# Kernel tuning notes

Hardware: AMD Instinct MI355X
Metric: run time of the kernel (lower is better)

## Reference

```python
import jax, jax.numpy as jnp
import numpy as np

B, N, C_IN = 4, 8192, 64
NPOINT, NSAMPLE = 2048, 32
RADIUS = 0.8


def fps(xyz, npoint):
    """Furthest point sampling. xyz: (B, N, 3) -> (B, npoint) int32 indices."""
    b, n, _ = xyz.shape
    init_idx = jnp.zeros((b,), jnp.int32)
    dists0 = jnp.full((b, n), 1e10, xyz.dtype)

    def body(carry, _):
        dists, last = carry
        p = xyz[jnp.arange(b), last]                      # (B, 3) last selected point
        d = jnp.sum((xyz - p[:, None, :]) ** 2, axis=-1)  # (B, N)
        dists = jnp.minimum(dists, d)
        nxt = jnp.argmax(dists, axis=-1).astype(jnp.int32)
        return (dists, nxt), nxt

    (_, _), rest = jax.lax.scan(body, (dists0, init_idx), None, length=npoint - 1)
    return jnp.concatenate([init_idx[None, :], rest], axis=0).T  # (B, npoint)


def setup_inputs() -> dict:
    key = jax.random.key(0)
    k = jax.random.split(key, 4)
    xyz = jax.random.normal(k[0], (B, N, 3), jnp.float32) * 3.0   # point coords
    features = jax.random.normal(k[1], (B, C_IN, N), jnp.float32)
    w1 = jax.random.normal(k[2], (128, C_IN + 3), jnp.float32) * 0.05
    b1 = jnp.zeros((128,), jnp.float32)
    w2 = jax.random.normal(k[3], (256, 128), jnp.float32) * 0.05
    b2 = jnp.zeros((256,), jnp.float32)
    return {"xyz": xyz, "features": features, "w1": w1, "b1": b1, "w2": w2, "b2": b2}


def reference(xyz, features, w1, b1, w2, b2):
    b, n, _ = xyz.shape
    # --- d-fps sampling + gather_operation(new_xyz) ---
    idx_fps = fps(xyz, NPOINT)                                  # (B, S)
    new_xyz = jax.vmap(lambda p, i: p[i])(xyz, idx_fps)         # (B, S, 3)

    # --- ball query (QueryAndGroup): first NSAMPLE points within RADIUS ---
    d2 = jnp.sum((new_xyz[:, :, None, :] - xyz[:, None, :, :]) ** 2, -1)  # (B, S, N)
    in_ball = d2 < RADIUS ** 2
    idx_cnt = jnp.sum(in_ball, axis=-1)                          # (B, S)
    score = jnp.where(in_ball, jnp.arange(n, dtype=jnp.int32), n)
    neg_vals, _ = jax.lax.top_k(-score, NSAMPLE)
    idx = -neg_vals                                              # (B, S, ns) smallest valid indices
    valid = idx < n
    first = jnp.where(valid[..., :1], idx[..., :1], 0)           # pad empties with first hit (or 0)
    idx = jnp.where(valid, idx, first)

    # --- group: relative xyz concat features (use_xyz=True) ---
    gxyz = jax.vmap(lambda p, i: p[i])(xyz, idx)                 # (B, S, ns, 3)
    rel = (gxyz - new_xyz[:, :, None, :]).transpose(0, 3, 1, 2)  # (B, 3, S, ns)
    gfeat = jax.vmap(lambda f, i: f[:, i])(features, idx)        # (B, C, S, ns)
    g = jnp.concatenate([rel, gfeat], axis=1)                    # (B, C+3, S, ns)
    g = g * (idx_cnt > 0).astype(g.dtype)[:, None, :, None]      # zero empty balls

    # --- shared point MLP (1x1 conv stack) + max pool over samples ---
    h = jax.nn.relu(jnp.einsum('oc,bcsn->bosn', w1, g) + b1[None, :, None, None])
    h = jax.nn.relu(jnp.einsum('oc,bcsn->bosn', w2, h) + b2[None, :, None, None])
    pooled = jnp.max(h, axis=-1)                                 # (B, 256, S)
    return new_xyz, pooled
```

## Files before the change

### kernel.cpp

```cpp
#include <hip/hip_runtime.h>

#define NPTS   8192
#define NPT    2048
#define NS     32
#define CIN    64
#define BATCH  4
#define R2     0.64f

#define NWORK  252
#define NQUAD  2048

__global__ __launch_bounds__(256) void prep_kernel(const float* __restrict__ w1,
                                                   const float* __restrict__ w2,
                                                   float* __restrict__ w1t,
                                                   float* __restrict__ w2t) {
  int i = blockIdx.x * 256 + threadIdx.x;
  if (i < 128 * 67) {
    int o = i / 67, c = i % 67;
    w1t[c * 128 + o] = w1[i];
  }
  if (i < 256 * 128) {
    int o = i >> 7, c = i & 127;
    w2t[c * 256 + o] = w2[i];
  }
}

__global__ __launch_bounds__(256) void prep_t_kernel(const float* __restrict__ feat,
                                                     float* __restrict__ FT) {
  const int b = blockIdx.x >> 7;
  const int n0 = (blockIdx.x & 127) << 6;
  const int tid = threadIdx.x;
  __shared__ float T[64][65];

  const float* F = feat + (size_t)b * CIN * NPTS;
#pragma unroll
  for (int p = 0; p < 16; ++p) {
    int c = p * 4 + (tid >> 6), ln = tid & 63;
    T[c][ln] = F[(size_t)c * NPTS + n0 + ln];
  }
  __syncthreads();
  float* O = FT + (size_t)b * NPTS * CIN;
#pragma unroll
  for (int p = 0; p < 4; ++p) {
    int j = tid >> 2, q = (tid & 3) + p * 4;
    float4 v = make_float4(T[q * 4 + 0][j], T[q * 4 + 1][j],
                           T[q * 4 + 2][j], T[q * 4 + 3][j]);
    *(float4*)&O[(size_t)(n0 + j) * CIN + q * 4] = v;
  }
}

__device__ inline uint32_t part1by2(uint32_t x) {
  x &= 1023u;
  x = (x | (x << 16)) & 0x030000FFu;
  x = (x | (x << 8))  & 0x0300F00Fu;
  x = (x | (x << 4))  & 0x030C30C3u;
  x = (x | (x << 2))  & 0x09249249u;
  return x;
}

__device__ inline uint32_t morton3(float x, float y, float z) {
  int qx = (int)((x + 16.f) * 32.f);
  int qy = (int)((y + 16.f) * 32.f);
  int qz = (int)((z + 16.f) * 32.f);
  qx = qx < 0 ? 0 : (qx > 1023 ? 1023 : qx);
  qy = qy < 0 ? 0 : (qy > 1023 ? 1023 : qy);
  qz = qz < 0 ? 0 : (qz > 1023 ? 1023 : qz);
  return part1by2((uint32_t)qx) | (part1by2((uint32_t)qy) << 1) | (part1by2((uint32_t)qz) << 2);
}

__global__ __launch_bounds__(1024) void sort_kernel(const float* __restrict__ xyz,
                                                    float4* __restrict__ sorted) {
  const int b = blockIdx.x;
  const int tid = threadIdx.x;
  const float* X = xyz + (size_t)b * NPTS * 3;
  __shared__ uint32_t S[NPTS];

  for (int k = 0; k < 8; ++k) {
    int p = tid + (k << 10);
    uint32_t m = morton3(X[p * 3 + 0], X[p * 3 + 1], X[p * 3 + 2]);
    S[p] = ((m >> 11) << 13) | (uint32_t)p;
  }
  __syncthreads();
  for (unsigned k = 2; k <= NPTS; k <<= 1) {
    for (unsigned j = k >> 1; j > 0; j >>= 1) {
      for (int i = tid; i < NPTS; i += 1024) {
        int l = i ^ (int)j;
        if (l > i) {
          uint32_t a = S[i], c = S[l];
          bool sw = ((i & k) == 0) ? (a > c) : (a < c);
          if (sw) { S[i] = c; S[l] = a; }
        }
      }
      __syncthreads();
    }
  }
  for (int k = 0; k < 8; ++k) {
    int pos = tid + (k << 10);
    int o = (int)(S[pos] & 8191u);
    float4 v;
    v.x = X[o * 3 + 0]; v.y = X[o * 3 + 1]; v.z = X[o * 3 + 2];
    v.w = __int_as_float(o);
    sorted[(size_t)b * NPTS + pos] = v;
  }
}


#define DPP_ROR_U32_MAX(v)                                                       \
  {                                                                              \
    uint32_t _t;                                                                 \
    _t = (uint32_t)__builtin_amdgcn_update_dpp(0, (int)(v), 0x121, 0xF, 0xF, false); if (_t > (v)) (v) = _t; \
    _t = (uint32_t)__builtin_amdgcn_update_dpp(0, (int)(v), 0x122, 0xF, 0xF, false); if (_t > (v)) (v) = _t; \
    _t = (uint32_t)__builtin_amdgcn_update_dpp(0, (int)(v), 0x124, 0xF, 0xF, false); if (_t > (v)) (v) = _t; \
    _t = (uint32_t)__builtin_amdgcn_update_dpp(0, (int)(v), 0x128, 0xF, 0xF, false); if (_t > (v)) (v) = _t; \
  }

#define DPP_ROR_U32_MIN(v)                                                       \
  {                                                                              \
    uint32_t _t;                                                                 \
    _t = (uint32_t)__builtin_amdgcn_update_dpp(-1, (int)(v), 0x121, 0xF, 0xF, false); if (_t < (v)) (v) = _t; \
    _t = (uint32_t)__builtin_amdgcn_update_dpp(-1, (int)(v), 0x122, 0xF, 0xF, false); if (_t < (v)) (v) = _t; \
    _t = (uint32_t)__builtin_amdgcn_update_dpp(-1, (int)(v), 0x124, 0xF, 0xF, false); if (_t < (v)) (v) = _t; \
    _t = (uint32_t)__builtin_amdgcn_update_dpp(-1, (int)(v), 0x128, 0xF, 0xF, false); if (_t < (v)) (v) = _t; \
  }

#define CSWAP(i, j)                                                              \
  if (oid[i] > oid[j]) {                                                         \
    int _ti = oid[i]; oid[i] = oid[j]; oid[j] = _ti;                             \
    float _tf;                                                                   \
    _tf = px[i]; px[i] = px[j]; px[j] = _tf;                                     \
    _tf = py[i]; py[i] = py[j]; py[j] = _tf;                                     \
    _tf = pz[i]; pz[i] = pz[j]; pz[j] = _tf;                                     \
  }

__global__ __launch_bounds__(1024, 1) void fused_kernel(
    const float* __restrict__ xyz, const float4* __restrict__ sorted,
    const float* __restrict__ FT,
    const float* __restrict__ w1t, const float* __restrict__ b1,
    const float* __restrict__ w2t, const float* __restrict__ b2,
    float* __restrict__ new_xyz, float* __restrict__ pooled,
    int* __restrict__ progress) {
  const int tid = threadIdx.x;
  const int lane = tid & 63;
  const int wv = tid >> 6;

  __shared__ __align__(16) char SM[100416];

  if (blockIdx.x < 4) {
    const int b = blockIdx.x;
    float* XL = (float*)SM;
    uint2 (*rec)[16] = (uint2(*)[16])(SM + 98304);
    const float* X = xyz + (size_t)b * NPTS * 3;
    const float4* SP = sorted + (size_t)b * NPTS;

    for (int i = tid; i < NPTS * 3; i += 1024) XL[i] = X[i];

    float px[8], py[8], pz[8], dmin[8];
    int oid[8];
#pragma unroll
    for (int k = 0; k < 8; ++k) {
      float4 p = SP[tid * 8 + k];
      px[k] = p.x; py[k] = p.y; pz[k] = p.z;
      oid[k] = __float_as_int(p.w);
      dmin[k] = 1e10f;
    }
    CSWAP(0, 1) CSWAP(2, 3) CSWAP(4, 5) CSWAP(6, 7)
    CSWAP(0, 2) CSWAP(1, 3) CSWAP(4, 6) CSWAP(5, 7)
    CSWAP(1, 2) CSWAP(5, 6)
    CSWAP(0, 4) CSWAP(1, 5) CSWAP(2, 6) CSWAP(3, 7)
    CSWAP(2, 4) CSWAP(3, 5)
    CSWAP(1, 2) CSWAP(3, 4) CSWAP(5, 6)

    float bxmin = px[0], bxmax = px[0], bymin = py[0], bymax = py[0], bzmin = pz[0], bzmax = pz[0];
#pragma unroll
    for (int k = 1; k < 8; ++k) {
      bxmin = fminf(bxmin, px[k]); bxmax = fmaxf(bxmax, px[k]);
      bymin = fminf(bymin, py[k]); bymax = fmaxf(bymax, py[k]);
      bzmin = fminf(bzmin, pz[k]); bzmax = fmaxf(bzmax, pz[k]);
    }
    float cmaxv = 1e10f;
    int   cmaxi = oid[0];
    uint32_t wwm = 0u, wwi = 0u;

    float cx = X[0], cy = X[1], cz = X[2];
    if (tid == 0) {
      new_xyz[(size_t)b * NPT * 3 + 0] = cx;
      new_xyz[(size_t)b * NPT * 3 + 1] = cy;
      new_xyz[(size_t)b * NPT * 3 + 2] = cz;
    }
    __syncthreads();

    for (int t = 1; t < NPT; ++t) {
      float ex = fmaxf(fmaxf(bxmin - cx, cx - bxmax), 0.f);
      float ey = fmaxf(fmaxf(bymin - cy, cy - bymax), 0.f);
      float ez = fmaxf(fmaxf(bzmin - cz, cz - bzmax), 0.f);
      float dlb = (ex * ex + ey * ey + ez * ez) * 0.9999f;
      bool act = dlb < cmaxv;

      if (__ballot(act)) {
        if (act) {
          float mv = -1.0f; int mi = 0;
#pragma unroll
          for (int k = 0; k < 8; ++k) {
            float dx = px[k] - cx, dy = py[k] - cy, dz = pz[k] - cz;
            float d = __fadd_rn(__fadd_rn(__fmul_rn(dx, dx), __fmul_rn(dy, dy)), __fmul_rn(dz, dz));
            float dm = fminf(dmin[k], d);
            dmin[k] = dm;
            if (dm > mv) { mv = dm; mi = oid[k]; }
          }
          cmaxv = mv; cmaxi = mi;
        }
        uint32_t vb = __float_as_uint(cmaxv);
        uint32_t rm = vb;
        DPP_ROR_U32_MAX(rm)
        uint32_t m0 = (uint32_t)__builtin_amdgcn_readlane((int)rm, 0);
        uint32_t m1 = (uint32_t)__builtin_amdgcn_readlane((int)rm, 16);
        uint32_t m2 = (uint32_t)__builtin_amdgcn_readlane((int)rm, 32);
        uint32_t m3 = (uint32_t)__builtin_amdgcn_readlane((int)rm, 48);
        uint32_t wm = m0 > m1 ? m0 : m1;
        uint32_t wmb = m2 > m3 ? m2 : m3;
        wm = wm > wmb ? wm : wmb;
        unsigned long long em = __ballot(vb == wm);
        uint32_t wi;
        if (__popcll(em) == 1) {
          wi = (uint32_t)__builtin_amdgcn_readlane(cmaxi, __ffsll(em) - 1);
        } else {
          uint32_t ik = (vb == wm) ? (uint32_t)cmaxi : 0xFFFFFFFFu;
          DPP_ROR_U32_MIN(ik)
          uint32_t i0 = (uint32_t)__builtin_amdgcn_readlane((int)ik, 0);
          uint32_t i1 = (uint32_t)__builtin_amdgcn_readlane((int)ik, 16);
          uint32_t i2 = (uint32_t)__builtin_amdgcn_readlane((int)ik, 32);
          uint32_t i3 = (uint32_t)__builtin_amdgcn_readlane((int)ik, 48);
          wi = i0 < i1 ? i0 : i1;
          uint32_t wib = i2 < i3 ? i2 : i3;
          wi = wi < wib ? wi : wib;
        }
        wwm = wm; wwi = wi;
      }

      const int buf = t & 1;
      if (lane == 0) { rec[buf][wv].x = wwm; rec[buf][wv].y = wwi; }
      __syncthreads();

      uint2 r = rec[buf][lane & 15];
      uint32_t bm = r.x;
      DPP_ROR_U32_MAX(bm)
      uint32_t ci = (r.x == bm) ? r.y : 0xFFFFFFFFu;
      DPP_ROR_U32_MIN(ci)
      int sidx = __builtin_amdgcn_readfirstlane((int)ci);

      cx = XL[3 * sidx + 0];
      cy = XL[3 * sidx + 1];
      cz = XL[3 * sidx + 2];

      if (tid == 0) {
        float* o = new_xyz + ((size_t)b * NPT + t) * 3;
        o[0] = cx; o[1] = cy; o[2] = cz;
        if ((t & 15) == 15)
          __hip_atomic_store(progress + b, t, __ATOMIC_RELEASE, __HIP_MEMORY_SCOPE_AGENT);
      }
    }
  } else {
    float* G    = (float*)SM;
    float* H1   = (float*)(SM + 34304);
    int*   lidx = (int*)(SM + 99840);
    float* ctr  = (float*)(SM + 100352);

    const int wbid = blockIdx.x - 4;

    for (int qg = wbid; qg < NQUAD; qg += NWORK) {
      const int b = qg & 3;
      const int s0 = (qg >> 2) * 4;
      const float* X  = xyz + (size_t)b * NPTS * 3;
      const float* Fp = FT + (size_t)b * NPTS * CIN;

      if (tid == 0) {
        while (__hip_atomic_load(progress + b, __ATOMIC_ACQUIRE, __HIP_MEMORY_SCOPE_AGENT) < s0 + 3)
          __builtin_amdgcn_s_sleep(2);
      }
      __syncthreads();

      if (tid < 12) ctr[tid] = new_xyz[((size_t)b * NPT + s0) * 3 + tid];
      if (wv < 4) {
        const int s = s0 + wv;
        const float cx = new_xyz[((size_t)b * NPT + s) * 3 + 0];
        const float cy = new_xyz[((size_t)b * NPT + s) * 3 + 1];
        const float cz = new_xyz[((size_t)b * NPT + s) * 3 + 2];
        int* out = lidx + wv * NS;
        int found = 0;
        int first = -1;
        for (int base = 0; base < NPTS; base += 64) {
          const int p = base + lane;
          float x = X[p * 3 + 0], y = X[p * 3 + 1], z = X[p * 3 + 2];
          float dx = x - cx, dy = y - cy, dz = z - cz;
          float d2 = __fadd_rn(__fadd_rn(__fmul_rn(dx, dx), __fmul_rn(dy, dy)), __fmul_rn(dz, dz));
          unsigned long long mask = __ballot(d2 < R2);
          if (mask != 0ull && first < 0) first = base + __ffsll((unsigned long long)mask) - 1;
          if (found < NS) {
            if ((mask >> lane) & 1ull) {
              int rank = found + __popcll(mask & ((1ull << lane) - 1ull));
              if (rank < NS) out[rank] = p;
            }
          }
          found += __popcll(mask);
          if (found >= NS) break;
        }
        if (found < NS) {
          int pad = (first < 0) ? 0 : first;
          if (lane >= found && lane < NS) out[lane] = pad;
        }
      }
      __syncthreads();

      {
        int j = tid >> 3, q = tid & 7;
        int p = lidx[j];
        const float4* row = (const float4*)(Fp + (size_t)p * CIN);
        float4 v0 = row[q * 2 + 0];
        float4 v1 = row[q * 2 + 1];
        float vs[8] = {v0.x, v0.y, v0.z, v0.w, v1.x, v1.y, v1.z, v1.w};
#pragma unroll
        for (int i = 0; i < 8; ++i)
          G[(3 + q * 8 + i) * 128 + j] = vs[i];
      }
      if (tid < 384) {
        int c = tid >> 7, j = tid & 127;
        int p = lidx[j];
        G[c * 128 + j] = X[p * 3 + c] - ctr[(j >> 5) * 3 + c];
      }
      __syncthreads();

      {
        const int oi = tid >> 5, ji = tid & 31;
        const int o0 = oi * 4, j0 = ji * 4;
        float acc[4][4];
#pragma unroll
        for (int i = 0; i < 4; ++i)
#pragma unroll
          for (int jj = 0; jj < 4; ++jj) acc[i][jj] = 0.f;
#pragma unroll 4
        for (int c = 0; c < 67; ++c) {
          float4 g  = *(const float4*)&G[c * 128 + j0];
          float4 wf = *(const float4*)&w1t[c * 128 + o0];
          float ga[4] = {g.x, g.y, g.z, g.w};
          float wa[4] = {wf.x, wf.y, wf.z, wf.w};
#pragma unroll
          for (int i = 0; i < 4; ++i)
#pragma unroll
            for (int jj = 0; jj < 4; ++jj)
              acc[i][jj] = fmaf(wa[i], ga[jj], acc[i][jj]);
        }
        float4 bb = *(const float4*)&b1[o0];
        float ba[4] = {bb.x, bb.y, bb.z, bb.w};
#pragma unroll
        for (int i = 0; i < 4; ++i) {
          float4 h;
          h.x = fmaxf(acc[i][0] + ba[i], 0.f);
          h.y = fmaxf(acc[i][1] + ba[i], 0.f);
          h.z = fmaxf(acc[i][2] + ba[i], 0.f);
          h.w = fmaxf(acc[i][3] + ba[i], 0.f);
          *(float4*)&H1[(o0 + i) * 128 + j0] = h;
        }
      }
      __syncthreads();

      {
        const int oi = tid >> 5, ji = tid & 31;
        const int o0 = oi * 8, j0 = ji * 4;
        float acc[8][4];
#pragma unroll
        for (int i = 0; i < 8; ++i)
#pragma unroll
          for (int jj = 0; jj < 4; ++jj) acc[i][jj] = 0.f;
#pragma unroll 2
        for (int c = 0; c < 128; ++c) {
          float4 h  = *(const float4*)&H1[c * 128 + j0];
          float4 wa4 = *(const float4*)&w2t[c * 256 + o0];
          float4 wb4 = *(const float4*)&w2t[c * 256 + o0 + 4];
          float ha[4] = {h.x, h.y, h.z, h.w};
          float wa[8] = {wa4.x, wa4.y, wa4.z, wa4.w, wb4.x, wb4.y, wb4.z, wb4.w};
#pragma unroll
          for (int i = 0; i < 8; ++i)
#pragma unroll
            for (int jj = 0; jj < 4; ++jj)
              acc[i][jj] = fmaf(wa[i], ha[jj], acc[i][jj]);
        }
        float4 b2a = *(const float4*)&b2[o0];
        float4 b2b = *(const float4*)&b2[o0 + 4];
        float bb[8] = {b2a.x, b2a.y, b2a.z, b2a.w, b2b.x, b2b.y, b2b.z, b2b.w};
        float m[8];
#pragma unroll
        for (int i = 0; i < 8; ++i) {
          float v0 = fmaxf(acc[i][0] + bb[i], 0.f);
          float v1 = fmaxf(acc[i][1] + bb[i], 0.f);
          float v2 = fmaxf(acc[i][2] + bb[i], 0.f);
          float v3 = fmaxf(acc[i][3] + bb[i], 0.f);
          m[i] = fmaxf(fmaxf(v0, v1), fmaxf(v2, v3));
        }
#pragma unroll
        for (int off = 1; off < 8; off <<= 1)
#pragma unroll
          for (int i = 0; i < 8; ++i) m[i] = fmaxf(m[i], __shfl_xor(m[i], off));
        if ((ji & 7) == 0) {
          int sidx = s0 + (ji >> 3);
#pragma unroll
          for (int i = 0; i < 8; ++i)
            pooled[((size_t)b * 256 + o0 + i) * (size_t)NPT + sidx] = m[i];
        }
      }
    }
  }
}

extern "C" void kernel_launch(void* const* d_in, const int* in_sizes, int n_in,
                              void* d_out, int out_size, void* d_ws, size_t ws_size,
                              hipStream_t stream) {
  (void)in_sizes; (void)n_in; (void)out_size; (void)ws_size;
  const float* xyz  = (const float*)d_in[0];
  const float* feat = (const float*)d_in[1];
  const float* w1   = (const float*)d_in[2];
  const float* b1   = (const float*)d_in[3];
  const float* w2   = (const float*)d_in[4];
  const float* b2   = (const float*)d_in[5];

  float* out     = (float*)d_out;
  float* new_xyz = out;
  float* pooled  = out + (size_t)BATCH * NPT * 3;

  char* ws = (char*)d_ws;
  float*  w1t      = (float*)ws;
  float*  w2t      = (float*)(ws + 34304);
  float4* sorted   = (float4*)(ws + 165376);
  float*  FT       = (float*)(ws + 689664);
  int*    progress = (int*)(ws + 9078272);

  prep_kernel<<<128, 256, 0, stream>>>(w1, w2, w1t, w2t);
  prep_t_kernel<<<BATCH * 128, 256, 0, stream>>>(feat, FT);
  sort_kernel<<<BATCH, 1024, 0, stream>>>(xyz, sorted);
  (void)hipMemsetAsync(progress, 0, 16, stream);
  fused_kernel<<<256, 1024, 0, stream>>>(xyz, sorted, FT, w1t, b1, w2t, b2,
                                         new_xyz, pooled, progress);
}
```

Measured before the change: 1.685 ms.

## Add wave-level bounding-box skip and broadcast winner coords via LDS records

In the FPS blocks, each wave now computes a wave-wide bounding box and skips the whole per-thread check and the wave reduction when that box cannot beat the wave's previous max. The winning lane also writes its point coordinates into a small per-wave LDS record, and the next centre is picked out of those records with readlane. This replaces the indexed lookup into a 96KB copy of xyz held in LDS, which is removed along with its initial load. The cost is more bookkeeping per iteration, and the correctness of the skip depends on the stale wave max staying a valid bound.

```diff
diff --git a/kernel.cpp b/kernel.cpp
--- a/kernel.cpp
+++ b/kernel.cpp
@@ -147,12 +147,10 @@
 
   if (blockIdx.x < 4) {
     const int b = blockIdx.x;
-    float* XL = (float*)SM;
-    uint2 (*rec)[16] = (uint2(*)[16])(SM + 98304);
+    uint2  (*rec)[16]  = (uint2(*)[16])(SM + 98304);
+    float4 (*recc)[16] = (float4(*)[16])(SM + 98560);
     const float* X = xyz + (size_t)b * NPTS * 3;
     const float4* SP = sorted + (size_t)b * NPTS;
-
-    for (int i = tid; i < NPTS * 3; i += 1024) XL[i] = X[i];
 
     float px[8], py[8], pz[8], dmin[8];
     int oid[8];
@@ -177,9 +175,25 @@
       bymin = fminf(bymin, py[k]); bymax = fmaxf(bymax, py[k]);
       bzmin = fminf(bzmin, pz[k]); bzmax = fmaxf(bzmax, pz[k]);
     }
+    float wbxmin = bxmin, wbxmax = bxmax;
+    float wbymin = bymin, wbymax = bymax;
+    float wbzmin = bzmin, wbzmax = bzmax;
+#pragma unroll
+    for (int off = 1; off < 64; off <<= 1) {
+      wbxmin = fminf(wbxmin, __shfl_xor(wbxmin, off));
+      wbxmax = fmaxf(wbxmax, __shfl_xor(wbxmax, off));
+      wbymin = fminf(wbymin, __shfl_xor(wbymin, off));
+      wbymax = fmaxf(wbymax, __shfl_xor(wbymax, off));
+      wbzmin = fminf(wbzmin, __shfl_xor(wbzmin, off));
+      wbzmax = fmaxf(wbzmax, __shfl_xor(wbzmax, off));
+    }
+
     float cmaxv = 1e10f;
     int   cmaxi = oid[0];
     uint32_t wwm = 0u, wwi = 0u;
+    float wwmf = 1e10f;
+    bool  iswin = false;
+    float wwx = 0.f, wwy = 0.f, wwz = 0.f;
 
     float cx = X[0], cy = X[1], cz = X[2];
     if (tid == 0) {
@@ -190,67 +204,83 @@
     __syncthreads();
 
     for (int t = 1; t < NPT; ++t) {
-      float ex = fmaxf(fmaxf(bxmin - cx, cx - bxmax), 0.f);
-      float ey = fmaxf(fmaxf(bymin - cy, cy - bymax), 0.f);
-      float ez = fmaxf(fmaxf(bzmin - cz, cz - bzmax), 0.f);
-      float dlb = (ex * ex + ey * ey + ez * ez) * 0.9999f;
-      bool act = dlb < cmaxv;
-
-      if (__ballot(act)) {
-        if (act) {
-          float mv = -1.0f; int mi = 0;
-#pragma unroll
-          for (int k = 0; k < 8; ++k) {
-            float dx = px[k] - cx, dy = py[k] - cy, dz = pz[k] - cz;
-            float d = __fadd_rn(__fadd_rn(__fmul_rn(dx, dx), __fmul_rn(dy, dy)), __fmul_rn(dz, dz));
-            float dm = fminf(dmin[k], d);
-            dmin[k] = dm;
-            if (dm > mv) { mv = dm; mi = oid[k]; }
+      float exw = fmaxf(fmaxf(wbxmin - cx, cx - wbxmax), 0.f);
+      float eyw = fmaxf(fmaxf(wbymin - cy, cy - wbymax), 0.f);
+      float ezw = fmaxf(fmaxf(wbzmin - cz, cz - wbzmax), 0.f);
+      float dlbw = (exw * exw + eyw * eyw + ezw * ezw) * 0.9999f;
+
+      if (dlbw < wwmf) {
+        float ex = fmaxf(fmaxf(bxmin - cx, cx - bxmax), 0.f);
+        float ey = fmaxf(fmaxf(bymin - cy, cy - bymax), 0.f);
+        float ez = fmaxf(fmaxf(bzmin - cz, cz - bzmax), 0.f);
+        float dlb = (ex * ex + ey * ey + ez * ez) * 0.9999f;
+        bool act = dlb < cmaxv;
+
+        if (__ballot(act)) {
+          if (act) {
+            float mv = -1.0f; int mi = 0;
+#pragma unroll
+            for (int k = 0; k < 8; ++k) {
+              float dx = px[k] - cx, dy = py[k] - cy, dz = pz[k] - cz;
+              float d = __fadd_rn(__fadd_rn(__fmul_rn(dx, dx), __fmul_rn(dy, dy)), __fmul_rn(dz, dz));
+              float dm = fminf(dmin[k], d);
+              dmin[k] = dm;
+              if (dm > mv) { mv = dm; mi = oid[k]; }
+            }
+            cmaxv = mv; cmaxi = mi;
           }
-          cmaxv = mv; cmaxi = mi;
-        }
-        uint32_t vb = __float_as_uint(cmaxv);
-        uint32_t rm = vb;
-        DPP_ROR_U32_MAX(rm)
-        uint32_t m0 = (uint32_t)__builtin_amdgcn_readlane((int)rm, 0);
-        uint32_t m1 = (uint32_t)__builtin_amdgcn_readlane((int)rm, 16);
-        uint32_t m2 = (uint32_t)__builtin_amdgcn_readlane((int)rm, 32);
-        uint32_t m3 = (uint32_t)__builtin_amdgcn_readlane((int)rm, 48);
-        uint32_t wm = m0 > m1 ? m0 : m1;
-        uint32_t wmb = m2 > m3 ? m2 : m3;
-        wm = wm > wmb ? wm : wmb;
-        unsigned long long em = __ballot(vb == wm);
-        uint32_t wi;
-        if (__popcll(em) == 1) {
-          wi = (uint32_t)__builtin_amdgcn_readlane(cmaxi, __ffsll(em) - 1);
-        } else {
-          uint32_t ik = (vb == wm) ? (uint32_t)cmaxi : 0xFFFFFFFFu;
-          DPP_ROR_U32_MIN(ik)
-          uint32_t i0 = (uint32_t)__builtin_amdgcn_readlane((int)ik, 0);
-          uint32_t i1 = (uint32_t)__builtin_amdgcn_readlane((int)ik, 16);
-          uint32_t i2 = (uint32_t)__builtin_amdgcn_readlane((int)ik, 32);
-          uint32_t i3 = (uint32_t)__builtin_amdgcn_readlane((int)ik, 48);
-          wi = i0 < i1 ? i0 : i1;
-          uint32_t wib = i2 < i3 ? i2 : i3;
-          wi = wi < wib ? wi : wib;
-        }
-        wwm = wm; wwi = wi;
+          uint32_t vb = __float_as_uint(cmaxv);
+          uint32_t rm = vb;
+          DPP_ROR_U32_MAX(rm)
+          uint32_t m0 = (uint32_t)__builtin_amdgcn_readlane((int)rm, 0);
+          uint32_t m1 = (uint32_t)__builtin_amdgcn_readlane((int)rm, 16);
+          uint32_t m2 = (uint32_t)__builtin_amdgcn_readlane((int)rm, 32);
+          uint32_t m3 = (uint32_t)__builtin_amdgcn_readlane((int)rm, 48);
+          uint32_t wm = m0 > m1 ? m0 : m1;
+          uint32_t wmb = m2 > m3 ? m2 : m3;
+          wm = wm > wmb ? wm : wmb;
+          unsigned long long em = __ballot(vb == wm);
+          uint32_t wi;
+          if (__popcll(em) == 1) {
+            wi = (uint32_t)__builtin_amdgcn_readlane(cmaxi, __ffsll(em) - 1);
+          } else {
+            uint32_t ik = (vb == wm) ? (uint32_t)cmaxi : 0xFFFFFFFFu;
+            DPP_ROR_U32_MIN(ik)
+            uint32_t i0 = (uint32_t)__builtin_amdgcn_readlane((int)ik, 0);
+            uint32_t i1 = (uint32_t)__builtin_amdgcn_readlane((int)ik, 16);
+            uint32_t i2 = (uint32_t)__builtin_amdgcn_readlane((int)ik, 32);
+            uint32_t i3 = (uint32_t)__builtin_amdgcn_readlane((int)ik, 48);
+            wi = i0 < i1 ? i0 : i1;
+            uint32_t wib = i2 < i3 ? i2 : i3;
+            wi = wi < wib ? wi : wib;
+          }
+          wwm = wm; wwi = wi;
+          wwmf = __uint_as_float(wm);
+          iswin = (vb == wm) && ((uint32_t)cmaxi == wi);
+          if (iswin) {
+#pragma unroll
+            for (int k = 0; k < 8; ++k)
+              if (oid[k] == (int)wi) { wwx = px[k]; wwy = py[k]; wwz = pz[k]; }
+          }
+        }
       }
 
       const int buf = t & 1;
       if (lane == 0) { rec[buf][wv].x = wwm; rec[buf][wv].y = wwi; }
-      __syncthreads();
-
-      uint2 r = rec[buf][lane & 15];
+      if (iswin)     { recc[buf][wv] = make_float4(wwx, wwy, wwz, 0.f); }
+      __syncthreads();
+
+      uint2  r  = rec[buf][lane & 15];
+      float4 rc = recc[buf][lane & 15];
       uint32_t bm = r.x;
       DPP_ROR_U32_MAX(bm)
-      uint32_t ci = (r.x == bm) ? r.y : 0xFFFFFFFFu;
+      uint32_t ci = (r.x == bm) ? ((r.y << 4) | (uint32_t)(lane & 15)) : 0xFFFFFFFFu;
       DPP_ROR_U32_MIN(ci)
-      int sidx = __builtin_amdgcn_readfirstlane((int)ci);
-
-      cx = XL[3 * sidx + 0];
-      cy = XL[3 * sidx + 1];
-      cz = XL[3 * sidx + 2];
+      int s = __builtin_amdgcn_readfirstlane((int)ci);
+      int wl = s & 15;
+      cx = __int_as_float(__builtin_amdgcn_readlane(__float_as_int(rc.x), wl));
+      cy = __int_as_float(__builtin_amdgcn_readlane(__float_as_int(rc.y), wl));
+      cz = __int_as_float(__builtin_amdgcn_readlane(__float_as_int(rc.z), wl));
 
       if (tid == 0) {
         float* o = new_xyz + ((size_t)b * NPT + t) * 3;
```

Result: slower. 2.558 ms (+51.8%).

## Fold prep, transpose and Morton sort kernels into the persistent fused kernel

Applied to the files above, without the earlier changes.

Removes three separate launches by moving the weight transpose and feature transpose into the worker blocks and the Morton bitonic sort into the FPS blocks, using shared memory instead of a global sorted buffer. Worker blocks synchronize on a global counter before consuming FT. FPS results are staged in a shared ring and flushed to global memory every 16 steps. This cuts launch overhead and lets the sort overlap with the transposes, at the cost of more shared memory per block and a grid-wide spin barrier that assumes all blocks are co-resident.

```diff
diff --git a/kernel.cpp b/kernel.cpp
--- a/kernel.cpp
+++ b/kernel.cpp
@@ -9,45 +9,6 @@
 
 #define NWORK  252
 #define NQUAD  2048
-
-__global__ __launch_bounds__(256) void prep_kernel(const float* __restrict__ w1,
-                                                   const float* __restrict__ w2,
-                                                   float* __restrict__ w1t,
-                                                   float* __restrict__ w2t) {
-  int i = blockIdx.x * 256 + threadIdx.x;
-  if (i < 128 * 67) {
-    int o = i / 67, c = i % 67;
-    w1t[c * 128 + o] = w1[i];
-  }
-  if (i < 256 * 128) {
-    int o = i >> 7, c = i & 127;
-    w2t[c * 256 + o] = w2[i];
-  }
-}
-
-__global__ __launch_bounds__(256) void prep_t_kernel(const float* __restrict__ feat,
-                                                     float* __restrict__ FT) {
-  const int b = blockIdx.x >> 7;
-  const int n0 = (blockIdx.x & 127) << 6;
-  const int tid = threadIdx.x;
-  __shared__ float T[64][65];
-
-  const float* F = feat + (size_t)b * CIN * NPTS;
-#pragma unroll
-  for (int p = 0; p < 16; ++p) {
-    int c = p * 4 + (tid >> 6), ln = tid & 63;
-    T[c][ln] = F[(size_t)c * NPTS + n0 + ln];
-  }
-  __syncthreads();
-  float* O = FT + (size_t)b * NPTS * CIN;
-#pragma unroll
-  for (int p = 0; p < 4; ++p) {
-    int j = tid >> 2, q = (tid & 3) + p * 4;
-    float4 v = make_float4(T[q * 4 + 0][j], T[q * 4 + 1][j],
-                           T[q * 4 + 2][j], T[q * 4 + 3][j]);
-    *(float4*)&O[(size_t)(n0 + j) * CIN + q * 4] = v;
-  }
-}
 
 __device__ inline uint32_t part1by2(uint32_t x) {
   x &= 1023u;
@@ -68,42 +29,6 @@
   return part1by2((uint32_t)qx) | (part1by2((uint32_t)qy) << 1) | (part1by2((uint32_t)qz) << 2);
 }
 
-__global__ __launch_bounds__(1024) void sort_kernel(const float* __restrict__ xyz,
-                                                    float4* __restrict__ sorted) {
-  const int b = blockIdx.x;
-  const int tid = threadIdx.x;
-  const float* X = xyz + (size_t)b * NPTS * 3;
-  __shared__ uint32_t S[NPTS];
-
-  for (int k = 0; k < 8; ++k) {
-    int p = tid + (k << 10);
-    uint32_t m = morton3(X[p * 3 + 0], X[p * 3 + 1], X[p * 3 + 2]);
-    S[p] = ((m >> 11) << 13) | (uint32_t)p;
-  }
-  __syncthreads();
-  for (unsigned k = 2; k <= NPTS; k <<= 1) {
-    for (unsigned j = k >> 1; j > 0; j >>= 1) {
-      for (int i = tid; i < NPTS; i += 1024) {
-        int l = i ^ (int)j;
-        if (l > i) {
-          uint32_t a = S[i], c = S[l];
-          bool sw = ((i & k) == 0) ? (a > c) : (a < c);
-          if (sw) { S[i] = c; S[l] = a; }
-        }
-      }
-      __syncthreads();
-    }
-  }
-  for (int k = 0; k < 8; ++k) {
-    int pos = tid + (k << 10);
-    int o = (int)(S[pos] & 8191u);
-    float4 v;
-    v.x = X[o * 3 + 0]; v.y = X[o * 3 + 1]; v.z = X[o * 3 + 2];
-    v.w = __int_as_float(o);
-    sorted[(size_t)b * NPTS + pos] = v;
-  }
-}
-
 
 #define DPP_ROR_U32_MAX(v)                                                       \
   {                                                                              \
@@ -133,34 +58,57 @@
   }
 
 __global__ __launch_bounds__(1024, 1) void fused_kernel(
-    const float* __restrict__ xyz, const float4* __restrict__ sorted,
-    const float* __restrict__ FT,
-    const float* __restrict__ w1t, const float* __restrict__ b1,
-    const float* __restrict__ w2t, const float* __restrict__ b2,
+    const float* __restrict__ xyz, const float* __restrict__ feat,
+    const float* __restrict__ w1, const float* __restrict__ b1,
+    const float* __restrict__ w2, const float* __restrict__ b2,
+    float* __restrict__ w1t, float* __restrict__ w2t,
+    float* __restrict__ FT,
     float* __restrict__ new_xyz, float* __restrict__ pooled,
     int* __restrict__ progress) {
   const int tid = threadIdx.x;
   const int lane = tid & 63;
   const int wv = tid >> 6;
-
-  __shared__ __align__(16) char SM[100416];
+  int* ftflag = progress + 4;
+
+  __shared__ __align__(16) char SM[131520];
 
   if (blockIdx.x < 4) {
     const int b = blockIdx.x;
-    float* XL = (float*)SM;
-    uint2 (*rec)[16] = (uint2(*)[16])(SM + 98304);
+    float*     XL  = (float*)SM;
+    uint32_t*  S   = (uint32_t*)(SM + 98304);
+    uint2 (*rec)[16] = (uint2(*)[16])(SM + 131072);
+    float*     ring = (float*)(SM + 131328);
     const float* X = xyz + (size_t)b * NPTS * 3;
-    const float4* SP = sorted + (size_t)b * NPTS;
 
     for (int i = tid; i < NPTS * 3; i += 1024) XL[i] = X[i];
+    __syncthreads();
+    for (int k = 0; k < 8; ++k) {
+      int p = tid + (k << 10);
+      uint32_t m = morton3(XL[p * 3 + 0], XL[p * 3 + 1], XL[p * 3 + 2]);
+      S[p] = ((m >> 11) << 13) | (uint32_t)p;
+    }
+    __syncthreads();
+    for (unsigned kk = 2; kk <= NPTS; kk <<= 1) {
+      for (unsigned j = kk >> 1; j > 0; j >>= 1) {
+        for (int i = tid; i < NPTS; i += 1024) {
+          int l = i ^ (int)j;
+          if (l > i) {
+            uint32_t a = S[i], c = S[l];
+            bool sw = ((i & kk) == 0) ? (a > c) : (a < c);
+            if (sw) { S[i] = c; S[l] = a; }
+          }
+        }
+        __syncthreads();
+      }
+    }
 
     float px[8], py[8], pz[8], dmin[8];
     int oid[8];
 #pragma unroll
     for (int k = 0; k < 8; ++k) {
-      float4 p = SP[tid * 8 + k];
-      px[k] = p.x; py[k] = p.y; pz[k] = p.z;
-      oid[k] = __float_as_int(p.w);
+      int o = (int)(S[tid * 8 + k] & 8191u);
+      px[k] = XL[3 * o + 0]; py[k] = XL[3 * o + 1]; pz[k] = XL[3 * o + 2];
+      oid[k] = o;
       dmin[k] = 1e10f;
     }
     CSWAP(0, 1) CSWAP(2, 3) CSWAP(4, 5) CSWAP(6, 7)
@@ -181,13 +129,8 @@
     int   cmaxi = oid[0];
     uint32_t wwm = 0u, wwi = 0u;
 
-    float cx = X[0], cy = X[1], cz = X[2];
-    if (tid == 0) {
-      new_xyz[(size_t)b * NPT * 3 + 0] = cx;
-      new_xyz[(size_t)b * NPT * 3 + 1] = cy;
-      new_xyz[(size_t)b * NPT * 3 + 2] = cz;
-    }
-    __syncthreads();
+    float cx = XL[0], cy = XL[1], cz = XL[2];
+    if (tid == 0) { ring[0] = cx; ring[1] = cy; ring[2] = cz; }
 
     for (int t = 1; t < NPT; ++t) {
       float ex = fmaxf(fmaxf(bxmin - cx, cx - bxmax), 0.f);
@@ -253,10 +196,15 @@
       cz = XL[3 * sidx + 2];
 
       if (tid == 0) {
-        float* o = new_xyz + ((size_t)b * NPT + t) * 3;
-        o[0] = cx; o[1] = cy; o[2] = cz;
-        if ((t & 15) == 15)
+        float* rg = ring + (t & 15) * 3;
+        rg[0] = cx; rg[1] = cy; rg[2] = cz;
+        if ((t & 15) == 15) {
+          float4* dst = (float4*)(new_xyz + ((size_t)b * NPT + (t - 15)) * 3);
+          float4* src = (float4*)ring;
+#pragma unroll
+          for (int q = 0; q < 12; ++q) dst[q] = src[q];
           __hip_atomic_store(progress + b, t, __ATOMIC_RELEASE, __HIP_MEMORY_SCOPE_AGENT);
+        }
       }
     }
   } else {
@@ -266,6 +214,46 @@
     float* ctr  = (float*)(SM + 100352);
 
     const int wbid = blockIdx.x - 4;
+
+    {
+      if (wbid == 0) {
+        for (int i = tid; i < 128 * 67; i += 1024) {
+          int o = i / 67, c = i % 67;
+          w1t[c * 128 + o] = w1[i];
+        }
+        for (int i = tid; i < 256 * 128; i += 1024) {
+          int o = i >> 7, c = i & 127;
+          w2t[c * 256 + o] = w2[i];
+        }
+      }
+      float (*T)[65] = (float(*)[65])SM;
+      for (int tile = wbid; tile < 512; tile += NWORK) {
+        const int tb = tile >> 7;
+        const int n0 = (tile & 127) << 6;
+        const float* F = feat + (size_t)tb * CIN * NPTS;
+        float* O = FT + (size_t)tb * NPTS * CIN;
+#pragma unroll
+        for (int p = 0; p < 4; ++p) {
+          int c = p * 16 + (tid >> 6), ln = tid & 63;
+          T[c][ln] = F[(size_t)c * NPTS + n0 + ln];
+        }
+        __syncthreads();
+        {
+          int j = tid >> 4, q = tid & 15;
+          float4 v = make_float4(T[q * 4 + 0][j], T[q * 4 + 1][j],
+                                 T[q * 4 + 2][j], T[q * 4 + 3][j]);
+          *(float4*)&O[(size_t)(n0 + j) * CIN + q * 4] = v;
+        }
+        __syncthreads();
+      }
+      if (tid == 0)
+        (void)__hip_atomic_fetch_add(ftflag, 1, __ATOMIC_RELEASE, __HIP_MEMORY_SCOPE_AGENT);
+      if (tid == 0) {
+        while (__hip_atomic_load(ftflag, __ATOMIC_ACQUIRE, __HIP_MEMORY_SCOPE_AGENT) < NWORK)
+          __builtin_amdgcn_s_sleep(2);
+      }
+      __syncthreads();
+    }
 
     for (int qg = wbid; qg < NQUAD; qg += NWORK) {
       const int b = qg & 3;
@@ -427,16 +415,12 @@
   float* pooled  = out + (size_t)BATCH * NPT * 3;
 
   char* ws = (char*)d_ws;
-  float*  w1t      = (float*)ws;
-  float*  w2t      = (float*)(ws + 34304);
-  float4* sorted   = (float4*)(ws + 165376);
-  float*  FT       = (float*)(ws + 689664);
-  int*    progress = (int*)(ws + 9078272);
-
-  prep_kernel<<<128, 256, 0, stream>>>(w1, w2, w1t, w2t);
-  prep_t_kernel<<<BATCH * 128, 256, 0, stream>>>(feat, FT);
-  sort_kernel<<<BATCH, 1024, 0, stream>>>(xyz, sorted);
-  (void)hipMemsetAsync(progress, 0, 16, stream);
-  fused_kernel<<<256, 1024, 0, stream>>>(xyz, sorted, FT, w1t, b1, w2t, b2,
-                                         new_xyz, pooled, progress);
+  float* w1t      = (float*)ws;
+  float* w2t      = (float*)(ws + 34304);
+  float* FT       = (float*)(ws + 165376);
+  int*   progress = (int*)(ws + 8553984);
+
+  (void)hipMemsetAsync(progress, 0, 32, stream);
+  fused_kernel<<<256, 1024, 0, stream>>>(xyz, feat, w1, b1, w2, b2,
+                                         w1t, w2t, FT, new_xyz, pooled, progress);
 }
```

Result: no change. 1.704 ms (+1.1%).

## Halve fused kernel block size to 512 threads and double per-thread work

Applied to the files above, without the earlier changes.

Launches the fused kernel with 512 threads per block instead of 1024. Each FPS thread now holds 16 sorted points, merged with an extra sorting network, and the MLP stages compute twice as many output channels per thread. Per-wave FPS records are duplicated into 16 slots so the existing 16-lane reduction still works with 8 waves. The intent is to cut the per-iteration block barrier and reduction cost in the serial FPS loop and allow more blocks per CU. The cost is higher register pressure and less parallelism inside each block for the grouping/MLP phase.

```diff
diff --git a/kernel.cpp b/kernel.cpp
--- a/kernel.cpp
+++ b/kernel.cpp
@@ -132,7 +132,9 @@
     _tf = pz[i]; pz[i] = pz[j]; pz[j] = _tf;                                     \
   }
 
-__global__ __launch_bounds__(1024, 1) void fused_kernel(
+__global__ __launch_bounds__(512)
+__attribute__((amdgpu_waves_per_eu(2, 8)))
+void fused_kernel(
     const float* __restrict__ xyz, const float4* __restrict__ sorted,
     const float* __restrict__ FT,
     const float* __restrict__ w1t, const float* __restrict__ b1,
@@ -143,7 +145,7 @@
   const int lane = tid & 63;
   const int wv = tid >> 6;
 
-  __shared__ __align__(16) char SM[100416];
+  __shared__ __align__(16) char SM[100864];
 
   if (blockIdx.x < 4) {
     const int b = blockIdx.x;
@@ -152,16 +154,15 @@
     const float* X = xyz + (size_t)b * NPTS * 3;
     const float4* SP = sorted + (size_t)b * NPTS;
 
-    for (int i = tid; i < NPTS * 3; i += 1024) XL[i] = X[i];
-
-    float px[8], py[8], pz[8], dmin[8];
-    int oid[8];
-#pragma unroll
-    for (int k = 0; k < 8; ++k) {
-      float4 p = SP[tid * 8 + k];
+    for (int i = tid; i < NPTS * 3; i += 512) XL[i] = X[i];
+
+    float px[16], py[16], pz[16], dmin[16];
+    int oid[16];
+#pragma unroll
+    for (int k = 0; k < 16; ++k) {
+      float4 p = SP[tid * 16 + k];
       px[k] = p.x; py[k] = p.y; pz[k] = p.z;
       oid[k] = __float_as_int(p.w);
-      dmin[k] = 1e10f;
     }
     CSWAP(0, 1) CSWAP(2, 3) CSWAP(4, 5) CSWAP(6, 7)
     CSWAP(0, 2) CSWAP(1, 3) CSWAP(4, 6) CSWAP(5, 7)
@@ -170,9 +171,33 @@
     CSWAP(2, 4) CSWAP(3, 5)
     CSWAP(1, 2) CSWAP(3, 4) CSWAP(5, 6)
 
+    CSWAP(8, 9) CSWAP(10, 11) CSWAP(12, 13) CSWAP(14, 15)
+    CSWAP(8, 10) CSWAP(9, 11) CSWAP(12, 14) CSWAP(13, 15)
+    CSWAP(9, 10) CSWAP(13, 14)
+    CSWAP(8, 12) CSWAP(9, 13) CSWAP(10, 14) CSWAP(11, 15)
+    CSWAP(10, 12) CSWAP(11, 13)
+    CSWAP(9, 10) CSWAP(11, 12) CSWAP(13, 14)
+
+    CSWAP(0, 15) CSWAP(1, 14) CSWAP(2, 13) CSWAP(3, 12)
+    CSWAP(4, 11) CSWAP(5, 10) CSWAP(6, 9) CSWAP(7, 8)
+    CSWAP(0, 4) CSWAP(1, 5) CSWAP(2, 6) CSWAP(3, 7)
+    CSWAP(8, 12) CSWAP(9, 13) CSWAP(10, 14) CSWAP(11, 15)
+    CSWAP(0, 2) CSWAP(1, 3) CSWAP(4, 6) CSWAP(5, 7)
+    CSWAP(8, 10) CSWAP(9, 11) CSWAP(12, 14) CSWAP(13, 15)
+    CSWAP(0, 1) CSWAP(2, 3) CSWAP(4, 5) CSWAP(6, 7)
+    CSWAP(8, 9) CSWAP(10, 11) CSWAP(12, 13) CSWAP(14, 15)
+
+#pragma unroll
+    for (int k = 0; k < 16; ++k) {
+      asm volatile("" : "+v"(px[k]), "+v"(py[k]), "+v"(pz[k]), "+v"(oid[k]));
+    }
+
+#pragma unroll
+    for (int k = 0; k < 16; ++k) dmin[k] = 1e10f;
+
     float bxmin = px[0], bxmax = px[0], bymin = py[0], bymax = py[0], bzmin = pz[0], bzmax = pz[0];
 #pragma unroll
-    for (int k = 1; k < 8; ++k) {
+    for (int k = 1; k < 16; ++k) {
       bxmin = fminf(bxmin, px[k]); bxmax = fmaxf(bxmax, px[k]);
       bymin = fminf(bymin, py[k]); bymax = fmaxf(bymax, py[k]);
       bzmin = fminf(bzmin, pz[k]); bzmax = fmaxf(bzmax, pz[k]);
@@ -200,7 +225,7 @@
         if (act) {
           float mv = -1.0f; int mi = 0;
 #pragma unroll
-          for (int k = 0; k < 8; ++k) {
+          for (int k = 0; k < 16; ++k) {
             float dx = px[k] - cx, dy = py[k] - cy, dz = pz[k] - cz;
             float d = __fadd_rn(__fadd_rn(__fmul_rn(dx, dx), __fmul_rn(dy, dy)), __fmul_rn(dz, dz));
             float dm = fminf(dmin[k], d);
@@ -238,7 +263,10 @@
       }
 
       const int buf = t & 1;
-      if (lane == 0) { rec[buf][wv].x = wwm; rec[buf][wv].y = wwi; }
+      if (lane == 0) {
+        rec[buf][wv].x = wwm;     rec[buf][wv].y = wwi;
+        rec[buf][wv + 8].x = wwm; rec[buf][wv + 8].y = wwi;
+      }
       __syncthreads();
 
       uint2 r = rec[buf][lane & 15];
@@ -312,15 +340,17 @@
       __syncthreads();
 
       {
-        int j = tid >> 3, q = tid & 7;
+        int j = tid >> 2, q = tid & 3;
         int p = lidx[j];
         const float4* row = (const float4*)(Fp + (size_t)p * CIN);
-        float4 v0 = row[q * 2 + 0];
-        float4 v1 = row[q * 2 + 1];
-        float vs[8] = {v0.x, v0.y, v0.z, v0.w, v1.x, v1.y, v1.z, v1.w};
-#pragma unroll
-        for (int i = 0; i < 8; ++i)
-          G[(3 + q * 8 + i) * 128 + j] = vs[i];
+#pragma unroll
+        for (int h = 0; h < 4; ++h) {
+          float4 v = row[q * 4 + h];
+          G[(3 + q * 16 + h * 4 + 0) * 128 + j] = v.x;
+          G[(3 + q * 16 + h * 4 + 1) * 128 + j] = v.y;
+          G[(3 + q * 16 + h * 4 + 2) * 128 + j] = v.z;
+          G[(3 + q * 16 + h * 4 + 3) * 128 + j] = v.w;
+        }
       }
       if (tid < 384) {
         int c = tid >> 7, j = tid & 127;
@@ -331,28 +361,30 @@
 
       {
         const int oi = tid >> 5, ji = tid & 31;
-        const int o0 = oi * 4, j0 = ji * 4;
-        float acc[4][4];
-#pragma unroll
-        for (int i = 0; i < 4; ++i)
+        const int o0 = oi * 8, j0 = ji * 4;
+        float acc[8][4];
+#pragma unroll
+        for (int i = 0; i < 8; ++i)
 #pragma unroll
           for (int jj = 0; jj < 4; ++jj) acc[i][jj] = 0.f;
 #pragma unroll 4
         for (int c = 0; c < 67; ++c) {
           float4 g  = *(const float4*)&G[c * 128 + j0];
-          float4 wf = *(const float4*)&w1t[c * 128 + o0];
+          float4 wa4 = *(const float4*)&w1t[c * 128 + o0];
+          float4 wb4 = *(const float4*)&w1t[c * 128 + o0 + 4];
           float ga[4] = {g.x, g.y, g.z, g.w};
-          float wa[4] = {wf.x, wf.y, wf.z, wf.w};
-#pragma unroll
-          for (int i = 0; i < 4; ++i)
+          float wa[8] = {wa4.x, wa4.y, wa4.z, wa4.w, wb4.x, wb4.y, wb4.z, wb4.w};
+#pragma unroll
+          for (int i = 0; i < 8; ++i)
 #pragma unroll
             for (int jj = 0; jj < 4; ++jj)
               acc[i][jj] = fmaf(wa[i], ga[jj], acc[i][jj]);
         }
-        float4 bb = *(const float4*)&b1[o0];
-        float ba[4] = {bb.x, bb.y, bb.z, bb.w};
-#pragma unroll
-        for (int i = 0; i < 4; ++i) {
+        float4 ba4 = *(const float4*)&b1[o0];
+        float4 bb4 = *(const float4*)&b1[o0 + 4];
+        float ba[8] = {ba4.x, ba4.y, ba4.z, ba4.w, bb4.x, bb4.y, bb4.z, bb4.w};
+#pragma unroll
+        for (int i = 0; i < 8; ++i) {
           float4 h;
           h.x = fmaxf(acc[i][0] + ba[i], 0.f);
           h.y = fmaxf(acc[i][1] + ba[i], 0.f);
@@ -365,31 +397,37 @@
 
       {
         const int oi = tid >> 5, ji = tid & 31;
-        const int o0 = oi * 8, j0 = ji * 4;
-        float acc[8][4];
-#pragma unroll
-        for (int i = 0; i < 8; ++i)
+        const int o0 = oi * 16, j0 = ji * 4;
+        float acc[16][4];
+#pragma unroll
+        for (int i = 0; i < 16; ++i)
 #pragma unroll
           for (int jj = 0; jj < 4; ++jj) acc[i][jj] = 0.f;
 #pragma unroll 2
         for (int c = 0; c < 128; ++c) {
           float4 h  = *(const float4*)&H1[c * 128 + j0];
-          float4 wa4 = *(const float4*)&w2t[c * 256 + o0];
-          float4 wb4 = *(const float4*)&w2t[c * 256 + o0 + 4];
+          float4 w0 = *(const float4*)&w2t[c * 256 + o0];
+          float4 w1v = *(const float4*)&w2t[c * 256 + o0 + 4];
+          float4 w2v = *(const float4*)&w2t[c * 256 + o0 + 8];
+          float4 w3v = *(const float4*)&w2t[c * 256 + o0 + 12];
           float ha[4] = {h.x, h.y, h.z, h.w};
-          float wa[8] = {wa4.x, wa4.y, wa4.z, wa4.w, wb4.x, wb4.y, wb4.z, wb4.w};
-#pragma unroll
-          for (int i = 0; i < 8; ++i)
+          float wa[16] = {w0.x, w0.y, w0.z, w0.w, w1v.x, w1v.y, w1v.z, w1v.w,
+                          w2v.x, w2v.y, w2v.z, w2v.w, w3v.x, w3v.y, w3v.z, w3v.w};
+#pragma unroll
+          for (int i = 0; i < 16; ++i)
 #pragma unroll
             for (int jj = 0; jj < 4; ++jj)
               acc[i][jj] = fmaf(wa[i], ha[jj], acc[i][jj]);
         }
-        float4 b2a = *(const float4*)&b2[o0];
-        float4 b2b = *(const float4*)&b2[o0 + 4];
-        float bb[8] = {b2a.x, b2a.y, b2a.z, b2a.w, b2b.x, b2b.y, b2b.z, b2b.w};
-        float m[8];
-#pragma unroll
-        for (int i = 0; i < 8; ++i) {
+        float4 b0 = *(const float4*)&b2[o0];
+        float4 b1v = *(const float4*)&b2[o0 + 4];
+        float4 b2v = *(const float4*)&b2[o0 + 8];
+        float4 b3v = *(const float4*)&b2[o0 + 12];
+        float bb[16] = {b0.x, b0.y, b0.z, b0.w, b1v.x, b1v.y, b1v.z, b1v.w,
+                        b2v.x, b2v.y, b2v.z, b2v.w, b3v.x, b3v.y, b3v.z, b3v.w};
+        float m[16];
+#pragma unroll
+        for (int i = 0; i < 16; ++i) {
           float v0 = fmaxf(acc[i][0] + bb[i], 0.f);
           float v1 = fmaxf(acc[i][1] + bb[i], 0.f);
           float v2 = fmaxf(acc[i][2] + bb[i], 0.f);
@@ -399,11 +437,11 @@
 #pragma unroll
         for (int off = 1; off < 8; off <<= 1)
 #pragma unroll
-          for (int i = 0; i < 8; ++i) m[i] = fmaxf(m[i], __shfl_xor(m[i], off));
+          for (int i = 0; i < 16; ++i) m[i] = fmaxf(m[i], __shfl_xor(m[i], off));
         if ((ji & 7) == 0) {
           int sidx = s0 + (ji >> 3);
 #pragma unroll
-          for (int i = 0; i < 8; ++i)
+          for (int i = 0; i < 16; ++i)
             pooled[((size_t)b * 256 + o0 + i) * (size_t)NPT + sidx] = m[i];
         }
       }
@@ -437,6 +475,6 @@
   prep_t_kernel<<<BATCH * 128, 256, 0, stream>>>(feat, FT);
   sort_kernel<<<BATCH, 1024, 0, stream>>>(xyz, sorted);
   (void)hipMemsetAsync(progress, 0, 16, stream);
-  fused_kernel<<<256, 1024, 0, stream>>>(xyz, sorted, FT, w1t, b1, w2t, b2,
-                                         new_xyz, pooled, progress);
-}
+  fused_kernel<<<256, 512, 0, stream>>>(xyz, sorted, FT, w1t, b1, w2t, b2,
+                                        new_xyz, pooled, progress);
+}
```

Result: slower. 1.866 ms (+10.8%).
